# Kernel tuning notes

Hardware: AMD Instinct MI355X
Metric: run time of the kernel (lower is better)

The kernel has to match this reference:

```python
import jax, jax.numpy as jnp
import numpy as np

A = 1.0  # slope of hard sigmoid (init arg `a`)


def setup_inputs() -> dict:
    key = jax.random.key(0)
    ks = jax.random.split(key, 10)
    H, B, BOT, TOP = 1024, 4096, 1024, 1024
    stdv = 1.0 / np.sqrt(H)
    u = lambda k, shp: jax.random.uniform(k, shp, jnp.float32, -stdv, stdv)
    U_11 = u(ks[0], (4 * H + 1, H))
    U_21 = u(ks[1], (4 * H + 1, TOP))
    W_01 = u(ks[2], (4 * H + 1, BOT))
    bias = u(ks[3], (4 * H + 1,))
    c = jax.random.normal(ks[4], (H, B), jnp.float32) * 0.1
    h = jnp.tanh(jax.random.normal(ks[5], (H, B), jnp.float32))
    h_bottom = jnp.tanh(jax.random.normal(ks[6], (BOT, B), jnp.float32))
    h_top = jnp.tanh(jax.random.normal(ks[7], (TOP, B), jnp.float32))
    z = (jax.random.uniform(ks[8], (1, B)) > 0.5).astype(jnp.float32)
    z_bottom = (jax.random.uniform(ks[9], (1, B)) > 0.5).astype(jnp.float32)
    return dict(c=c, h_bottom=h_bottom, h=h, h_top=h_top, z=z,
                z_bottom=z_bottom, U_11=U_11, U_21=U_21, W_01=W_01, bias=bias)


def reference(c, h_bottom, h, h_top, z, z_bottom, U_11, U_21, W_01, bias):
    H = U_11.shape[1]
    # [4H+1, B] pre-activations: recurrent + gated top-down + gated bottom-up + bias
    f_s = (W_01 @ h_bottom
           + z * (U_21 @ h_top)
           + z_bottom * (U_11 @ h)
           + bias[:, None])
    f = jax.nn.sigmoid(f_s[0:H])
    i = jax.nn.sigmoid(f_s[H:2 * H])
    o = jax.nn.sigmoid(f_s[2 * H:3 * H])
    g = jnp.tanh(f_s[3 * H:4 * H])
    z_hat = jnp.clip((f_s[4 * H:4 * H + 1] * A + 1.0) / 2.0, 0.0, 1.0)  # hard_sigm
    one = 1.0
    c_new = (z * (i * g)
             + (one - z) * (one - z_bottom) * c
             + (one - z) * z_bottom * (f * c + i * g))
    tanh_c = jnp.tanh(c_new)
    h_new = (z * o * tanh_c
             + (one - z) * (one - z_bottom) * h
             + (one - z) * z_bottom * o * tanh_c)
    # straight-through binary boundary: forward step(z_hat>0.5), backward identity
    z_new = z_hat + jax.lax.stop_gradient((z_hat > 0.5).astype(z_hat.dtype) - z_hat)
    return h_new, c_new, z_new
```

## Files before the change

### kernel.cpp

```cpp
#include <hip/hip_runtime.h>
#include <hip/hip_bf16.h>
#include <math.h>

#define Hd   1024
#define Bsz  4096
#define Kc   3072

typedef unsigned short u16;
typedef __attribute__((ext_vector_type(8))) u16 u16x8;
typedef __attribute__((ext_vector_type(2))) u16 u16x2;
typedef __attribute__((ext_vector_type(4))) float f32x4;
typedef __attribute__((ext_vector_type(8))) short bf16x8;

__device__ inline u16 f2bf(float f) {
    __hip_bfloat16 h = __float2bfloat16(f);
    return *reinterpret_cast<u16*>(&h);
}

__device__ inline float sigm(float x) { return 1.0f / (1.0f + __expf(-x)); }

__device__ inline void gload16(const void* g, const void* s) {
    __builtin_amdgcn_global_load_lds(
        (const __attribute__((address_space(1))) void*)g,
        (__attribute__((address_space(3))) void*)s, 16, 0, 0);
}

#define BAR()   __builtin_amdgcn_s_barrier()
#define VMW0()  asm volatile("s_waitcnt vmcnt(0)" ::: "memory")
#define LGKM0() asm volatile("s_waitcnt lgkmcnt(0)" ::: "memory")
#define PRIO1() __builtin_amdgcn_s_setprio(1)
#define PRIO0() __builtin_amdgcn_s_setprio(0)

__global__ __launch_bounds__(256) void prep_A(const float* __restrict__ U11,
                                              const float* __restrict__ U21,
                                              const float* __restrict__ W01,
                                              u16* __restrict__ Ab,
                                              float* __restrict__ out) {
    if (blockIdx.x == 0) {
        float* outz = out + (size_t)2 * Hd * Bsz;
        for (int i = threadIdx.x; i < Bsz; i += 256) outz[i] = 0.0f;
    }
    int t = blockIdx.x * 256 + threadIdx.x;
    int row = t / 384;
    int kc = (t - row * 384) * 8;
    int r = row >> 2, gate = row & 3;
    int sel = kc >> 10;
    int k = kc & 1023;
    const float* src = (sel == 0) ? W01 : ((sel == 1) ? U21 : U11);
    const float4* p = reinterpret_cast<const float4*>(src + (size_t)(gate * Hd + r) * Hd + k);
    float4 v0 = p[0], v1 = p[1];
    u16x8 o;
    o[0] = f2bf(v0.x); o[1] = f2bf(v0.y); o[2] = f2bf(v0.z); o[3] = f2bf(v0.w);
    o[4] = f2bf(v1.x); o[5] = f2bf(v1.y); o[6] = f2bf(v1.z); o[7] = f2bf(v1.w);
    *reinterpret_cast<u16x8*>(Ab + (size_t)row * Kc + kc) = o;
}

__global__ __launch_bounds__(1024) void prep_perm(const float* __restrict__ z,
                                                  const float* __restrict__ zb,
                                                  int* __restrict__ n_of_slot,
                                                  int* __restrict__ slot_of_n,
                                                  int* __restrict__ meta) {
    __shared__ int wtot[16][4];
    __shared__ int wbase[16][4];
    __shared__ int gbase[4];
    const int t = threadIdx.x, lane = t & 63, wv = t >> 6;
    int g[4]; int cnt[4] = {0, 0, 0, 0};
    const int n0 = t * 4;
#pragma unroll
    for (int j = 0; j < 4; ++j) {
        float zv = z[n0 + j], zbv = zb[n0 + j];
        int gg = (zv != 0.f) ? (zbv != 0.f ? 3 : 1) : (zbv != 0.f ? 2 : 0);
        g[j] = gg; cnt[gg]++;
    }
    int incl[4];
#pragma unroll
    for (int q = 0; q < 4; ++q) incl[q] = cnt[q];
    for (int off = 1; off < 64; off <<= 1) {
#pragma unroll
        for (int q = 0; q < 4; ++q) {
            int vv = __shfl_up(incl[q], off, 64);
            if (lane >= off) incl[q] += vv;
        }
    }
    if (lane == 63) {
#pragma unroll
        for (int q = 0; q < 4; ++q) wtot[wv][q] = incl[q];
    }
    for (int s = t; s < 4864; s += 1024) n_of_slot[s] = -1;
    __syncthreads();
    if (t == 0) {
        int run[4] = {0, 0, 0, 0};
        for (int ww = 0; ww < 16; ++ww) {
#pragma unroll
            for (int q = 0; q < 4; ++q) { wbase[ww][q] = run[q]; run[q] += wtot[ww][q]; }
        }
        int t3 = (run[3] + 255) >> 8, t2c = (run[2] + 255) >> 8, t1c = (run[1] + 255) >> 8;
        gbase[3] = 0; gbase[2] = t3 << 8; gbase[1] = (t3 + t2c) << 8; gbase[0] = 0;
        int Ttot = t3 + t2c + t1c;
        meta[0] = Ttot; meta[1] = t3; meta[2] = t3 + t2c; meta[3] = Ttot << 5;
        meta[8] = 0;
    }
    __syncthreads();
    int off[4];
#pragma unroll
    for (int q = 0; q < 4; ++q) off[q] = wbase[wv][q] + incl[q] - cnt[q];
#pragma unroll
    for (int j = 0; j < 4; ++j) {
        int gg = g[j];
        int slot = (gg == 0) ? -1 : (gbase[gg] + off[gg]);
        off[gg]++;
        slot_of_n[n0 + j] = slot;
        if (slot >= 0) n_of_slot[slot] = n0 + j;
    }
}

__global__ __launch_bounds__(256) void prep_B(const float* __restrict__ hb,
                                              const float* __restrict__ ht,
                                              const float* __restrict__ hh,
                                              const float* __restrict__ z,
                                              const float* __restrict__ zb,
                                              const float* __restrict__ U11,
                                              const float* __restrict__ U21,
                                              const float* __restrict__ W01,
                                              const int* __restrict__ slot_of_n,
                                              u16* __restrict__ Bp,
                                              float* __restrict__ out) {
    __shared__ float tile[64][33];
    __shared__ float red[8][32];
    int n0 = blockIdx.x * 32;
    int kg0 = blockIdx.y * 64;
    int sel = kg0 >> 10;
    int k0 = kg0 & 1023;
    const float* src = (sel == 0) ? hb : ((sel == 1) ? ht : hh);
    const float* wsrc = (sel == 0) ? W01 : ((sel == 1) ? U21 : U11);
    int t = threadIdx.x, tx = t & 31, ty = t >> 5;
#pragma unroll
    for (int j = 0; j < 8; ++j) {
        int kk = ty * 8 + j;
        tile[kk][tx] = src[(size_t)(k0 + kk) * Bsz + n0 + tx];
    }
    __syncthreads();
    {
        int kp = t & 31, ny = t >> 5;
#pragma unroll
        for (int j = 0; j < 4; ++j) {
            int nl = ny * 4 + j;
            int n = n0 + nl;
            float zv = z[n], zbv = zb[n];
            int gg = (zv != 0.f) ? (zbv != 0.f ? 3 : 1) : (zbv != 0.f ? 2 : 0);
            bool need = (sel == 0) ? (gg != 0) : ((sel == 1) ? ((gg & 1) != 0) : (gg >= 2));
            int slot = slot_of_n[n];
            if (need && slot >= 0) {
                float s = (sel == 0) ? 1.0f : ((sel == 1) ? zv : zbv);
                u16x2 o;
                o[0] = f2bf(tile[kp * 2][nl] * s);
                o[1] = f2bf(tile[kp * 2 + 1][nl] * s);
                *reinterpret_cast<u16x2*>(Bp + (size_t)slot * Kc + kg0 + kp * 2) = o;
            }
        }
    }
    {
        int col = t & 31, seg = t >> 5;
        const float* w = wsrc + (size_t)4096 * 1024 + k0 + seg * 8;
        float p = 0.0f;
#pragma unroll
        for (int j = 0; j < 8; ++j) p += w[j] * tile[seg * 8 + j][col];
        red[seg][col] = p;
        __syncthreads();
        if (seg == 0) {
            float tot = 0.0f;
#pragma unroll
            for (int q = 0; q < 8; ++q) tot += red[q][col];
            int n = n0 + col;
            float sca = (sel == 0) ? 1.0f : ((sel == 1) ? z[n] : zb[n]);
            atomicAdd(out + (size_t)2 * Hd * Bsz + n, tot * sca);
        }
    }
}

__global__ __launch_bounds__(256) void copy_pass(const float* __restrict__ c_in,
                                                 const float* __restrict__ h_in,
                                                 const float* __restrict__ z,
                                                 const float* __restrict__ zb,
                                                 const float* __restrict__ bias,
                                                 float* __restrict__ out) {
    int i = blockIdx.x * 256 + threadIdx.x;
    if (i < Bsz) {
        float* outz = out + (size_t)2 * Hd * Bsz;
        float s = outz[i] + bias[4096];
        float zh = (s + 1.0f) * 0.5f;
        zh = fminf(fmaxf(zh, 0.0f), 1.0f);
        outz[i] = (zh > 0.5f) ? 1.0f : 0.0f;
    }
    int r = i >> 12, n = i & 4095;
    if (z[n] == 0.f && zb[n] == 0.f) {
        out[(size_t)r * Bsz + n] = h_in[(size_t)r * Bsz + n];
        out[(size_t)Hd * Bsz + (size_t)r * Bsz + n] = c_in[(size_t)r * Bsz + n];
    }
}

__global__ __launch_bounds__(512, 2) void gemm_fused(
    const u16* __restrict__ A, const u16* __restrict__ Bp,
    const int* __restrict__ n_of_slot, int* __restrict__ meta,
    const float* __restrict__ c_in, const float* __restrict__ bias,
    float* __restrict__ out) {
    extern __shared__ __align__(16) u16 smem[];
    u16* const As = smem;
    u16* const Bs = smem + 16384;
    int* const shi = (int*)(smem + 49152);

    const int t = threadIdx.x;
    const int w = t >> 6, l = t & 63;
    const int wm = w >> 2, wn = w & 3;
    const int srow = t >> 3;
    const int sgs  = (t & 7) ^ (srow & 7);
    const int fr = l & 15, fq = l >> 4, fkey = l & 7;

    const int Ttot = meta[0];
    const int t3 = meta[1], t32 = meta[2];
    const int items = meta[3];
    int* ctr = meta + 8;

    for (;;) {
        __syncthreads();
        if (t == 0) *shi = atomicAdd(ctr, 1);
        __syncthreads();
        const int item = *shi;
        if (item >= items) break;
        const int tile = item >> 5, mseg = item & 31;
        const int grp = (tile < t3) ? 3 : ((tile < t32) ? 2 : 1);
        const int NTg = (grp == 3) ? 48 : 32;

        const u16* Aitem = A  + (size_t)(mseg * 128 + srow) * Kc + sgs * 8;
        const u16* Bitem = Bp + ((size_t)tile * 256 + srow) * Kc + sgs * 8;

        f32x4 acc[4][4];
#pragma unroll
        for (int i = 0; i < 4; ++i)
#pragma unroll
            for (int j = 0; j < 4; ++j) acc[i][j] = (f32x4){0.f, 0.f, 0.f, 0.f};

        auto ktmap = [&](int kt) { return (grp == 2 && kt >= 16) ? kt + 16 : kt; };
        auto stage = [&](int p, int ktg) {
#pragma unroll
            for (int iss = 0; iss < 2; ++iss)
                gload16(Aitem + (size_t)(iss * 64) * Kc + ktg * 64,
                        As + p * 8192 + (iss * 64 + (w << 3)) * 64);
#pragma unroll
            for (int iss = 0; iss < 4; ++iss)
                gload16(Bitem + (size_t)(iss * 64) * Kc + ktg * 64,
                        Bs + p * 16384 + (iss * 64 + (w << 3)) * 64);
        };

        stage(0, ktmap(0));
        for (int tt = 0; tt < NTg; ++tt) {
            const int p = tt & 1;
            LGKM0(); VMW0(); BAR();
            if (tt + 1 < NTg) stage(p ^ 1, ktmap(tt + 1));
            bf16x8 aF[4][2], bF[4][2];
#pragma unroll
            for (int mi = 0; mi < 4; ++mi)
#pragma unroll
                for (int ks = 0; ks < 2; ++ks)
                    aF[mi][ks] = *reinterpret_cast<const bf16x8*>(
                        As + p * 8192 + (wm * 64 + mi * 16 + fr) * 64 +
                        ((((ks << 2) + fq) ^ fkey) << 3));
#pragma unroll
            for (int ni = 0; ni < 4; ++ni)
#pragma unroll
                for (int ks = 0; ks < 2; ++ks)
                    bF[ni][ks] = *reinterpret_cast<const bf16x8*>(
                        Bs + p * 16384 + (wn * 64 + ni * 16 + fr) * 64 +
                        ((((ks << 2) + fq) ^ fkey) << 3));
            PRIO1();
#pragma unroll
            for (int mi = 0; mi < 4; ++mi)
#pragma unroll
                for (int ni = 0; ni < 4; ++ni)
#pragma unroll
                    for (int ks = 0; ks < 2; ++ks)
                        acc[mi][ni] = __builtin_amdgcn_mfma_f32_16x16x32_bf16(
                            aF[mi][ks], bF[ni][ks], acc[mi][ni], 0, 0, 0);
            PRIO0();
        }

        int nsl[4];
#pragma unroll
        for (int ni = 0; ni < 4; ++ni)
            nsl[ni] = n_of_slot[tile * 256 + wn * 64 + ni * 16 + fr];
#pragma unroll
        for (int mi = 0; mi < 4; ++mi) {
            const int r = mseg * 32 + wm * 16 + mi * 4 + fq;
            const float b0 = bias[r], b1 = bias[Hd + r];
            const float b2 = bias[2 * Hd + r], b3 = bias[3 * Hd + r];
#pragma unroll
            for (int ni = 0; ni < 4; ++ni) {
                const int n = nsl[ni];
                if (n < 0) continue;
                f32x4 a = acc[mi][ni];
                float ig = sigm(a[1] + b1);
                float og = sigm(a[2] + b2);
                float gg = tanhf(a[3] + b3);
                float cn;
                if (grp == 2) {
                    float fg = sigm(a[0] + b0);
                    cn = fg * c_in[(size_t)r * Bsz + n] + ig * gg;
                } else {
                    cn = ig * gg;
                }
                float hn = og * tanhf(cn);
                out[(size_t)r * Bsz + n] = hn;
                out[(size_t)Hd * Bsz + (size_t)r * Bsz + n] = cn;
            }
        }
    }
}

extern "C" void kernel_launch(void* const* d_in, const int* in_sizes, int n_in,
                              void* d_out, int out_size, void* d_ws, size_t ws_size,
                              hipStream_t stream) {
    (void)in_sizes; (void)n_in; (void)out_size; (void)ws_size;
    const float* c    = (const float*)d_in[0];
    const float* hb   = (const float*)d_in[1];
    const float* h    = (const float*)d_in[2];
    const float* ht   = (const float*)d_in[3];
    const float* z    = (const float*)d_in[4];
    const float* zb   = (const float*)d_in[5];
    const float* U11  = (const float*)d_in[6];
    const float* U21  = (const float*)d_in[7];
    const float* W01  = (const float*)d_in[8];
    const float* bias = (const float*)d_in[9];
    float* out = (float*)d_out;

    char* wsb = (char*)d_ws;
    u16* Ab        = (u16*)wsb;
    u16* Bp        = (u16*)(wsb + (size_t)25165824);
    int* n_of_slot = (int*)(wsb + (size_t)55050240);
    int* slot_of_n = (int*)(wsb + (size_t)55069696);
    int* meta      = (int*)(wsb + (size_t)55086080);

    hipFuncSetAttribute(reinterpret_cast<const void*>(gemm_fused),
                        hipFuncAttributeMaxDynamicSharedMemorySize, 98432);

    prep_perm<<<1, 1024, 0, stream>>>(z, zb, n_of_slot, slot_of_n, meta);
    prep_A<<<6144, 256, 0, stream>>>(U11, U21, W01, Ab, out);
    prep_B<<<dim3(128, 48), 256, 0, stream>>>(hb, ht, h, z, zb, U11, U21, W01,
                                              slot_of_n, Bp, out);
    copy_pass<<<16384, 256, 0, stream>>>(c, h, z, zb, bias, out);
    gemm_fused<<<256, 512, 98432, stream>>>(Ab, Bp, n_of_slot, meta, c, bias, out);
}
```

Baseline: 143.8 us.

## Replace persistent atomic scheduler with static grid and quarter-staged K pipeline

Drops the persistent work-queue loop, where blocks grabbed items through an atomic counter, and launches one block per (tile, mseg) item with an early exit for unused tiles. The K loop is split into four quadrant phases. Each phase issues one slice of the next stage's global-to-LDS loads, uses partial vmcnt waits, and runs a quarter of the MFMAs, so loads overlap compute instead of draining fully each iteration. The warp-to-row mapping changes to match the quadrant layout. The risks are tail imbalance from the static grid, extra barriers per iteration, and 608 blocks that cover at most 19 tiles, relying on the tile count never exceeding that.

Measured after the change: 135.6 us. 1.06x faster.

```diff
diff --git a/kernel.cpp b/kernel.cpp
--- a/kernel.cpp
+++ b/kernel.cpp
@@ -26,8 +26,7 @@
 }
 
 #define BAR()   __builtin_amdgcn_s_barrier()
-#define VMW0()  asm volatile("s_waitcnt vmcnt(0)" ::: "memory")
-#define LGKM0() asm volatile("s_waitcnt lgkmcnt(0)" ::: "memory")
+#define VMW(n)  asm volatile("s_waitcnt vmcnt(" #n ")" ::: "memory")
 #define PRIO1() __builtin_amdgcn_s_setprio(1)
 #define PRIO0() __builtin_amdgcn_s_setprio(0)
 
@@ -97,8 +96,7 @@
         int t3 = (run[3] + 255) >> 8, t2c = (run[2] + 255) >> 8, t1c = (run[1] + 255) >> 8;
         gbase[3] = 0; gbase[2] = t3 << 8; gbase[1] = (t3 + t2c) << 8; gbase[0] = 0;
         int Ttot = t3 + t2c + t1c;
-        meta[0] = Ttot; meta[1] = t3; meta[2] = t3 + t2c; meta[3] = Ttot << 5;
-        meta[8] = 0;
+        meta[0] = Ttot; meta[1] = t3; meta[2] = t3 + t2c;
     }
     __syncthreads();
     int off[4];
@@ -201,119 +199,147 @@
 
 __global__ __launch_bounds__(512, 2) void gemm_fused(
     const u16* __restrict__ A, const u16* __restrict__ Bp,
-    const int* __restrict__ n_of_slot, int* __restrict__ meta,
+    const int* __restrict__ n_of_slot, const int* __restrict__ meta,
     const float* __restrict__ c_in, const float* __restrict__ bias,
     float* __restrict__ out) {
     extern __shared__ __align__(16) u16 smem[];
     u16* const As = smem;
     u16* const Bs = smem + 16384;
-    int* const shi = (int*)(smem + 49152);
+
+    const int Ttot = meta[0], t3 = meta[1], t32 = meta[2];
+    const int item = blockIdx.x;
+    const int tile = item >> 5, mseg = item & 31;
+    if (tile >= Ttot) return;
+    const int grp = (tile < t3) ? 3 : ((tile < t32) ? 2 : 1);
+    const int NTg = (grp == 3) ? 48 : 32;
+    const bool skipmid = (grp == 2);
 
     const int t = threadIdx.x;
     const int w = t >> 6, l = t & 63;
-    const int wm = w >> 2, wn = w & 3;
+    const int wr = w >> 2, wc = w & 3;
     const int srow = t >> 3;
     const int sgs  = (t & 7) ^ (srow & 7);
     const int fr = l & 15, fq = l >> 4, fkey = l & 7;
 
-    const int Ttot = meta[0];
-    const int t3 = meta[1], t32 = meta[2];
-    const int items = meta[3];
-    int* ctr = meta + 8;
-
-    for (;;) {
-        __syncthreads();
-        if (t == 0) *shi = atomicAdd(ctr, 1);
-        __syncthreads();
-        const int item = *shi;
-        if (item >= items) break;
-        const int tile = item >> 5, mseg = item & 31;
-        const int grp = (tile < t3) ? 3 : ((tile < t32) ? 2 : 1);
-        const int NTg = (grp == 3) ? 48 : 32;
-
-        const u16* Aitem = A  + (size_t)(mseg * 128 + srow) * Kc + sgs * 8;
-        const u16* Bitem = Bp + ((size_t)tile * 256 + srow) * Kc + sgs * 8;
-
-        f32x4 acc[4][4];
-#pragma unroll
-        for (int i = 0; i < 4; ++i)
-#pragma unroll
-            for (int j = 0; j < 4; ++j) acc[i][j] = (f32x4){0.f, 0.f, 0.f, 0.f};
-
-        auto ktmap = [&](int kt) { return (grp == 2 && kt >= 16) ? kt + 16 : kt; };
-        auto stage = [&](int p, int ktg) {
-#pragma unroll
-            for (int iss = 0; iss < 2; ++iss)
-                gload16(Aitem + (size_t)(iss * 64) * Kc + ktg * 64,
-                        As + p * 8192 + (iss * 64 + (w << 3)) * 64);
-#pragma unroll
-            for (int iss = 0; iss < 4; ++iss)
-                gload16(Bitem + (size_t)(iss * 64) * Kc + ktg * 64,
-                        Bs + p * 16384 + (iss * 64 + (w << 3)) * 64);
-        };
-
-        stage(0, ktmap(0));
-        for (int tt = 0; tt < NTg; ++tt) {
-            const int p = tt & 1;
-            LGKM0(); VMW0(); BAR();
-            if (tt + 1 < NTg) stage(p ^ 1, ktmap(tt + 1));
-            bf16x8 aF[4][2], bF[4][2];
-#pragma unroll
-            for (int mi = 0; mi < 4; ++mi)
-#pragma unroll
-                for (int ks = 0; ks < 2; ++ks)
-                    aF[mi][ks] = *reinterpret_cast<const bf16x8*>(
-                        As + p * 8192 + (wm * 64 + mi * 16 + fr) * 64 +
-                        ((((ks << 2) + fq) ^ fkey) << 3));
-#pragma unroll
-            for (int ni = 0; ni < 4; ++ni)
-#pragma unroll
-                for (int ks = 0; ks < 2; ++ks)
-                    bF[ni][ks] = *reinterpret_cast<const bf16x8*>(
-                        Bs + p * 16384 + (wn * 64 + ni * 16 + fr) * 64 +
-                        ((((ks << 2) + fq) ^ fkey) << 3));
-            PRIO1();
-#pragma unroll
-            for (int mi = 0; mi < 4; ++mi)
-#pragma unroll
-                for (int ni = 0; ni < 4; ++ni)
-#pragma unroll
-                    for (int ks = 0; ks < 2; ++ks)
-                        acc[mi][ni] = __builtin_amdgcn_mfma_f32_16x16x32_bf16(
-                            aF[mi][ks], bF[ni][ks], acc[mi][ni], 0, 0, 0);
-            PRIO0();
-        }
-
-        int nsl[4];
-#pragma unroll
-        for (int ni = 0; ni < 4; ++ni)
-            nsl[ni] = n_of_slot[tile * 256 + wn * 64 + ni * 16 + fr];
-#pragma unroll
-        for (int mi = 0; mi < 4; ++mi) {
-            const int r = mseg * 32 + wm * 16 + mi * 4 + fq;
-            const float b0 = bias[r], b1 = bias[Hd + r];
-            const float b2 = bias[2 * Hd + r], b3 = bias[3 * Hd + r];
-#pragma unroll
-            for (int ni = 0; ni < 4; ++ni) {
-                const int n = nsl[ni];
-                if (n < 0) continue;
-                f32x4 a = acc[mi][ni];
-                float ig = sigm(a[1] + b1);
-                float og = sigm(a[2] + b2);
-                float gg = tanhf(a[3] + b3);
-                float cn;
-                if (grp == 2) {
-                    float fg = sigm(a[0] + b0);
-                    cn = fg * c_in[(size_t)r * Bsz + n] + ig * gg;
-                } else {
-                    cn = ig * gg;
-                }
-                float hn = og * tanhf(cn);
-                out[(size_t)r * Bsz + n] = hn;
-                out[(size_t)Hd * Bsz + (size_t)r * Bsz + n] = cn;
+    const u16* gA = A  + (size_t)(mseg * 128 + srow) * Kc + sgs * 8;
+    const u16* gB = Bp + ((size_t)tile * 256 + srow) * Kc + sgs * 8;
+
+    f32x4 acc[4][4];
+#pragma unroll
+    for (int i = 0; i < 4; ++i)
+#pragma unroll
+        for (int j = 0; j < 4; ++j) acc[i][j] = (f32x4){0.f, 0.f, 0.f, 0.f};
+
+    auto ktmap = [&](int kt) { return (skipmid && kt >= 16) ? kt + 16 : kt; };
+    auto stageA = [&](int buf, int mh, int kt) {
+        const int ktg = ktmap(kt);
+        gload16(gA + (size_t)(mh * 64) * Kc + ktg * 64,
+                As + buf * 8192 + (mh * 64 + (w << 3)) * 64);
+    };
+    auto stageB = [&](int buf, int nh, int kt) {
+        const int ktg = ktmap(kt);
+#pragma unroll
+        for (int iss = 0; iss < 2; ++iss)
+            gload16(gB + (size_t)(nh * 128 + iss * 64) * Kc + ktg * 64,
+                    Bs + buf * 16384 + (nh * 128 + iss * 64 + (w << 3)) * 64);
+    };
+
+    bf16x8 aF[2][2][2];
+    bf16x8 bF[2][2][2];
+
+    auto readA = [&](int buf, int mh, int miL, int ks) -> bf16x8 {
+        int row = mh * 64 + wr * 32 + miL * 16 + fr;
+        int g = ((ks << 2) + fq) ^ fkey;
+        return *reinterpret_cast<const bf16x8*>(As + buf * 8192 + row * 64 + g * 8);
+    };
+    auto readB = [&](int buf, int nh, int niL, int ks) -> bf16x8 {
+        int row = nh * 128 + wc * 32 + niL * 16 + fr;
+        int g = ((ks << 2) + fq) ^ fkey;
+        return *reinterpret_cast<const bf16x8*>(Bs + buf * 16384 + row * 64 + g * 8);
+    };
+
+#define MFMAQ(mh, nh)                                                         \
+    PRIO1();                                                                  \
+    _Pragma("unroll")                                                         \
+    for (int miL = 0; miL < 2; ++miL)                                         \
+        _Pragma("unroll")                                                     \
+        for (int niL = 0; niL < 2; ++niL)                                     \
+            _Pragma("unroll")                                                 \
+            for (int ks = 0; ks < 2; ++ks)                                    \
+                acc[(mh)*2 + miL][(nh)*2 + niL] =                             \
+                    __builtin_amdgcn_mfma_f32_16x16x32_bf16(                  \
+                        aF[mh][miL][ks], bF[nh][niL][ks],                     \
+                        acc[(mh)*2 + miL][(nh)*2 + niL], 0, 0, 0);            \
+    PRIO0()
+
+    stageA(0, 0, 0); stageB(0, 0, 0); stageA(0, 1, 0); stageB(0, 1, 0);
+    VMW(3); BAR();
+
+    for (int T = 0; T < NTg; ++T) {
+        const int p = T & 1, q2 = p ^ 1;
+        const bool more = (T + 1 < NTg);
+#pragma unroll
+        for (int miL = 0; miL < 2; ++miL) {
+            aF[0][miL][0] = readA(p, 0, miL, 0); aF[0][miL][1] = readA(p, 0, miL, 1);
+        }
+#pragma unroll
+        for (int niL = 0; niL < 2; ++niL) {
+            bF[0][niL][0] = readB(p, 0, niL, 0); bF[0][niL][1] = readB(p, 0, niL, 1);
+        }
+        if (more) { stageA(q2, 0, T + 1); VMW(3); } else { VMW(2); }
+        BAR();
+        MFMAQ(0, 0);
+#pragma unroll
+        for (int miL = 0; miL < 2; ++miL) {
+            aF[1][miL][0] = readA(p, 1, miL, 0); aF[1][miL][1] = readA(p, 1, miL, 1);
+        }
+        if (more) { stageB(q2, 0, T + 1); VMW(3); } else { VMW(0); }
+        BAR();
+        MFMAQ(1, 0);
+#pragma unroll
+        for (int niL = 0; niL < 2; ++niL) {
+            bF[1][niL][0] = readB(p, 1, niL, 0); bF[1][niL][1] = readB(p, 1, niL, 1);
+        }
+        if (more) stageA(q2, 1, T + 1);
+        BAR();
+        MFMAQ(1, 1);
+        if (more) { stageB(q2, 1, T + 1); VMW(3); }
+        BAR();
+        MFMAQ(0, 1);
+    }
+
+    int nsl[4];
+#pragma unroll
+    for (int bj = 0; bj < 4; ++bj) {
+        int slot = tile * 256 + (bj >> 1) * 128 + wc * 32 + (bj & 1) * 16 + fr;
+        nsl[bj] = n_of_slot[slot];
+    }
+#pragma unroll
+    for (int ai = 0; ai < 4; ++ai) {
+        const int u = mseg * 32 + (ai >> 1) * 16 + wr * 8 + (ai & 1) * 4 + fq;
+        const float b0 = bias[u], b1 = bias[Hd + u];
+        const float b2 = bias[2 * Hd + u], b3 = bias[3 * Hd + u];
+#pragma unroll
+        for (int bj = 0; bj < 4; ++bj) {
+            const int n = nsl[bj];
+            if (n < 0) continue;
+            f32x4 a = acc[ai][bj];
+            float ig = sigm(a[1] + b1);
+            float og = sigm(a[2] + b2);
+            float gg = tanhf(a[3] + b3);
+            float cn;
+            if (grp == 2) {
+                float fg = sigm(a[0] + b0);
+                cn = fg * c_in[(size_t)u * Bsz + n] + ig * gg;
+            } else {
+                cn = ig * gg;
             }
-        }
-    }
+            float hn = og * tanhf(cn);
+            out[(size_t)u * Bsz + n] = hn;
+            out[(size_t)Hd * Bsz + (size_t)u * Bsz + n] = cn;
+        }
+    }
+#undef MFMAQ
 }
 
 extern "C" void kernel_launch(void* const* d_in, const int* in_sizes, int n_in,
@@ -340,12 +366,12 @@
     int* meta      = (int*)(wsb + (size_t)55086080);
 
     hipFuncSetAttribute(reinterpret_cast<const void*>(gemm_fused),
-                        hipFuncAttributeMaxDynamicSharedMemorySize, 98432);
+                        hipFuncAttributeMaxDynamicSharedMemorySize, 98304);
 
     prep_perm<<<1, 1024, 0, stream>>>(z, zb, n_of_slot, slot_of_n, meta);
     prep_A<<<6144, 256, 0, stream>>>(U11, U21, W01, Ab, out);
     prep_B<<<dim3(128, 48), 256, 0, stream>>>(hb, ht, h, z, zb, U11, U21, W01,
                                               slot_of_n, Bp, out);
     copy_pass<<<16384, 256, 0, stream>>>(c, h, z, zb, bias, out);
-    gemm_fused<<<256, 512, 98432, stream>>>(Ab, Bp, n_of_slot, meta, c, bias, out);
-}
+    gemm_fused<<<608, 512, 98304, stream>>>(Ab, Bp, n_of_slot, meta, c, bias, out);
+}
```
